# Kernel tuning notes

Measured on AMD Instinct MI355X. Metric: run time of the kernel, lower is better.

## Reference

```python
import jax, jax.numpy as jnp
import numpy as np

B = 524288  # number of mel frames
MEL = 128   # mel bins (hard-coded in module)
D = 64      # code dim
K = 128     # codebook size


def setup_inputs() -> dict:
    key = jax.random.key(0)
    ks = jax.random.split(key, 7)
    return {
        "mel_frame": jax.random.normal(ks[0], (B, MEL), dtype=jnp.float32),
        "W_in": jax.random.normal(ks[1], (D, MEL), dtype=jnp.float32) * 0.05,
        "b_in": jax.random.normal(ks[2], (D,), dtype=jnp.float32) * 0.05,
        "cb0": jax.random.normal(ks[3], (K, D), dtype=jnp.float32),
        "cb1": jax.random.normal(ks[4], (K, D), dtype=jnp.float32),
        "W_out": jax.random.normal(ks[5], (MEL, D), dtype=jnp.float32) * 0.05,
        "b_out": jax.random.normal(ks[6], (MEL,), dtype=jnp.float32) * 0.05,
    }


def reference(mel_frame, W_in, b_in, cb0, cb1, W_out, b_out):
    # encode: project mel -> d, then greedy residual VQ over 2 codebooks
    z = mel_frame @ W_in.T + b_in                      # (B, D)
    residual = z
    z_q = jnp.zeros_like(z)
    idxs = []
    for cb in (cb0, cb1):
        # squared L2 distance without materializing (B, K, D):
        # ||r - c||^2 = ||r||^2 - 2 r.c + ||c||^2  -> (B, K)
        dist = (
            jnp.sum(residual * residual, axis=-1, keepdims=True)
            - 2.0 * (residual @ cb.T)
            + jnp.sum(cb * cb, axis=-1)
        )
        ind = jnp.argmin(dist, axis=-1)                # (B,)
        code = cb[ind]                                 # gather chosen codes (B, D)
        residual = residual - code
        z_q = z_q + code
        idxs.append(ind)
    # decode: sum of selected codes -> project back to mel
    mel = z_q @ W_out.T + b_out                        # (B, MEL)
    return mel, jnp.stack(idxs, axis=-1)
```

## Files before the change

### kernel.cpp

```cpp
#include <hip/hip_runtime.h>
#include <hip/hip_bf16.h>

#define B_ROWS   524288
#define MEL_BINS 128
#define DIM      64
#define KCODES   128

#define WS_WT 0
#define WS_N0 (WS_WT + MEL_BINS*DIM)
#define WS_N1 (WS_N0 + KCODES)
#define WS_T0 (WS_N1 + KCODES)
#define WS_T1 (WS_T0 + KCODES*MEL_BINS)
#define WS_TOT (WS_T1 + KCODES*MEL_BINS)

__device__ __forceinline__ float np_pairwise64_sq(const float* v) {
#pragma clang fp contract(off)
    float r0 = v[0]*v[0], r1 = v[1]*v[1], r2 = v[2]*v[2], r3 = v[3]*v[3];
    float r4 = v[4]*v[4], r5 = v[5]*v[5], r6 = v[6]*v[6], r7 = v[7]*v[7];
#pragma unroll
    for (int i = 8; i < 64; i += 8) {
        r0 += v[i+0]*v[i+0]; r1 += v[i+1]*v[i+1];
        r2 += v[i+2]*v[i+2]; r3 += v[i+3]*v[i+3];
        r4 += v[i+4]*v[i+4]; r5 += v[i+5]*v[i+5];
        r6 += v[i+6]*v[i+6]; r7 += v[i+7]*v[i+7];
    }
    return ((r0 + r1) + (r2 + r3)) + ((r4 + r5) + (r6 + r7));
}

__global__ __launch_bounds__(256) void rvq_precomp(
    const float* __restrict__ W_in, const float* __restrict__ cb0,
    const float* __restrict__ cb1, const float* __restrict__ W_out,
    float* __restrict__ ws)
{
#pragma clang fp contract(off)
    float* WT = ws + WS_WT;
    float* n0 = ws + WS_N0;
    float* n1 = ws + WS_N1;
    float* T0 = ws + WS_T0;
    float* T1 = ws + WS_T1;

    int tid = blockIdx.x * 256 + threadIdx.x;
    if (tid < 16384) {
        int i = tid >> 7, m = tid & 127;
        double a = 0.0;
        for (int d = 0; d < DIM; ++d)
            a = fma((double)cb0[i*DIM + d], (double)W_out[m*DIM + d], a);
        T0[tid] = (float)a;
    } else if (tid < 32768) {
        int t = tid - 16384;
        int i = t >> 7, m = t & 127;
        double a = 0.0;
        for (int d = 0; d < DIM; ++d)
            a = fma((double)cb1[i*DIM + d], (double)W_out[m*DIM + d], a);
        T1[t] = (float)a;
    } else if (tid < 40960) {
        int t = tid - 32768;
        int j = t >> 6, d = t & 63;
        WT[t] = W_in[d*MEL_BINS + j];
    } else if (tid < 41216) {
        int t = tid - 40960;
        const float* cb = (t & 128) ? cb1 : cb0;
        float*       nn = (t & 128) ? n1  : n0;
        int k = t & 127;
        nn[k] = np_pairwise64_sq(cb + k*DIM);
    }
}

__global__ __launch_bounds__(256) void rvq_main(
    const float* __restrict__ mel,
    const float* __restrict__ b_in,
    const float* __restrict__ cb0,
    const float* __restrict__ cb1,
    const float* __restrict__ b_out,
    const float* __restrict__ ws,
    float* __restrict__ out_mel,
    float* __restrict__ out_idx)
{
#pragma clang fp contract(off)
    const float* __restrict__ n0 = ws + WS_N0;
    const float* __restrict__ n1 = ws + WS_N1;
    const float* __restrict__ T0 = ws + WS_T0;
    const float* __restrict__ T1 = ws + WS_T1;

    __shared__ float slds[8192];
    float4* s4 = reinterpret_cast<float4*>(slds);
    const float4* s4c = reinterpret_cast<const float4*>(slds);

    const int tid = threadIdx.x;
    const int b = blockIdx.x * 256 + tid;

    {
        const float4* src = reinterpret_cast<const float4*>(ws + WS_WT);
#pragma unroll
        for (int i = 0; i < 8; ++i) s4[i*256 + tid] = src[i*256 + tid];
    }
    __syncthreads();

    float z[DIM];
#pragma unroll
    for (int d = 0; d < DIM; ++d) z[d] = 0.f;

    const float4* melr = reinterpret_cast<const float4*>(mel + (size_t)b * MEL_BINS);
    for (int jc = 0; jc < MEL_BINS / 4; ++jc) {
        float4 m4 = melr[jc];
#pragma unroll
        for (int seg = 0; seg < 4; ++seg) {
            float mj = (seg == 0) ? m4.x : (seg == 1) ? m4.y : (seg == 2) ? m4.z : m4.w;
            const float4* w4 = s4c + (jc*4 + seg)*16;
#pragma unroll
            for (int q = 0; q < 16; ++q) {
                float4 wv = w4[q];
                z[4*q + 0] = fmaf(wv.x, mj, z[4*q + 0]);
                z[4*q + 1] = fmaf(wv.y, mj, z[4*q + 1]);
                z[4*q + 2] = fmaf(wv.z, mj, z[4*q + 2]);
                z[4*q + 3] = fmaf(wv.w, mj, z[4*q + 3]);
            }
        }
    }
#pragma unroll
    for (int d = 0; d < DIM; ++d) z[d] = z[d] + b_in[d];

    float s0 = z[0]*z[0], s1 = z[1]*z[1], s2 = z[2]*z[2], s3 = z[3]*z[3];
    float s4r = z[4]*z[4], s5 = z[5]*z[5], s6 = z[6]*z[6], s7 = z[7]*z[7];
#pragma unroll
    for (int i = 8; i < 64; i += 8) {
        s0 += z[i+0]*z[i+0]; s1 += z[i+1]*z[i+1];
        s2 += z[i+2]*z[i+2]; s3 += z[i+3]*z[i+3];
        s4r += z[i+4]*z[i+4]; s5 += z[i+5]*z[i+5];
        s6 += z[i+6]*z[i+6]; s7 += z[i+7]*z[i+7];
    }
    float sum_rr = ((s0 + s1) + (s2 + s3)) + ((s4r + s5) + (s6 + s7));

    __syncthreads();
    {
        const float4* src = reinterpret_cast<const float4*>(cb0);
#pragma unroll
        for (int i = 0; i < 8; ++i) s4[i*256 + tid] = src[i*256 + tid];
    }
    __syncthreads();

    float best0 = 3.4e38f; int i0 = 0;
    for (int k = 0; k < KCODES; ++k) {
        const float4* c4 = s4c + k*16;
        float acc = 0.f;
#pragma unroll
        for (int q = 0; q < 16; ++q) {
            float4 cv = c4[q];
            acc = fmaf(cv.x, z[4*q + 0], acc);
            acc = fmaf(cv.y, z[4*q + 1], acc);
            acc = fmaf(cv.z, z[4*q + 2], acc);
            acc = fmaf(cv.w, z[4*q + 3], acc);
        }
        float dist = (sum_rr - 2.0f*acc) + n0[k];
        if (dist < best0) { best0 = dist; i0 = k; }
    }

    __syncthreads();
    {
        const float4* src = reinterpret_cast<const float4*>(cb1);
#pragma unroll
        for (int i = 0; i < 8; ++i) s4[i*256 + tid] = src[i*256 + tid];
    }

    {
        const float* c = cb0 + (size_t)i0 * DIM;
#pragma unroll
        for (int d = 0; d < DIM; ++d) z[d] = z[d] - c[d];
    }

    s0 = z[0]*z[0]; s1 = z[1]*z[1]; s2 = z[2]*z[2]; s3 = z[3]*z[3];
    s4r = z[4]*z[4]; s5 = z[5]*z[5]; s6 = z[6]*z[6]; s7 = z[7]*z[7];
#pragma unroll
    for (int i = 8; i < 64; i += 8) {
        s0 += z[i+0]*z[i+0]; s1 += z[i+1]*z[i+1];
        s2 += z[i+2]*z[i+2]; s3 += z[i+3]*z[i+3];
        s4r += z[i+4]*z[i+4]; s5 += z[i+5]*z[i+5];
        s6 += z[i+6]*z[i+6]; s7 += z[i+7]*z[i+7];
    }
    sum_rr = ((s0 + s1) + (s2 + s3)) + ((s4r + s5) + (s6 + s7));

    __syncthreads();

    float best1 = 3.4e38f; int i1 = 0;
    for (int k = 0; k < KCODES; ++k) {
        const float4* c4 = s4c + k*16;
        float acc = 0.f;
#pragma unroll
        for (int q = 0; q < 16; ++q) {
            float4 cv = c4[q];
            acc = fmaf(cv.x, z[4*q + 0], acc);
            acc = fmaf(cv.y, z[4*q + 1], acc);
            acc = fmaf(cv.z, z[4*q + 2], acc);
            acc = fmaf(cv.w, z[4*q + 3], acc);
        }
        float dist = (sum_rr - 2.0f*acc) + n1[k];
        if (dist < best1) { best1 = dist; i1 = k; }
    }

    const float4* t0r = reinterpret_cast<const float4*>(T0 + (size_t)i0 * MEL_BINS);
    const float4* t1r = reinterpret_cast<const float4*>(T1 + (size_t)i1 * MEL_BINS);
    float4* outr = reinterpret_cast<float4*>(out_mel + (size_t)b * MEL_BINS);
#pragma unroll 4
    for (int q = 0; q < MEL_BINS / 4; ++q) {
        float4 a = t0r[q], c = t1r[q];
        float4 o;
        o.x = a.x + c.x + b_out[4*q + 0];
        o.y = a.y + c.y + b_out[4*q + 1];
        o.z = a.z + c.z + b_out[4*q + 2];
        o.w = a.w + c.w + b_out[4*q + 3];
        outr[q] = o;
    }

    out_idx[2*(size_t)b + 0] = (float)i0;
    out_idx[2*(size_t)b + 1] = (float)i1;
}

extern "C" void kernel_launch(void* const* d_in, const int* in_sizes, int n_in,
                              void* d_out, int out_size, void* d_ws, size_t ws_size,
                              hipStream_t stream)
{
    const float* mel   = (const float*)d_in[0];
    const float* W_in  = (const float*)d_in[1];
    const float* b_in  = (const float*)d_in[2];
    const float* cb0   = (const float*)d_in[3];
    const float* cb1   = (const float*)d_in[4];
    const float* W_out = (const float*)d_in[5];
    const float* b_out = (const float*)d_in[6];

    float* ws      = (float*)d_ws;
    float* out_mel = (float*)d_out;
    float* out_idx = (float*)d_out + (size_t)B_ROWS * MEL_BINS;

    rvq_precomp<<<(WS_TOT + 255) / 256, 256, 0, stream>>>(W_in, cb0, cb1, W_out, ws);
    rvq_main<<<B_ROWS / 256, 256, 0, stream>>>(mel, b_in, cb0, cb1, b_out, ws,
                                               out_mel, out_idx);
}
```

Measured before the change: 570.1 us.

## Compute VQ distances with split-bf16 MFMA and exact fp32 rescoring of candidates

Replaces the per-thread scalar 128-code distance loops with wave-level MFMA matrix multiplies. Residuals and codebooks are split into bf16 hi/lo parts (three MFMA products), and codebooks are stored in a swizzled LDS table. A bitmask of codes within a small margin of the approximate minimum is built by shuffles, and only those candidates are rescored in exact fp32 from global memory. This removes most scalar FMA work, at the cost of many bpermutes and shuffles, divergent rescoring loops, and a fixed margin that must cover the bf16 error.

```diff
diff --git a/kernel.cpp b/kernel.cpp
--- a/kernel.cpp
+++ b/kernel.cpp
@@ -5,6 +5,10 @@
 #define MEL_BINS 128
 #define DIM      64
 #define KCODES   128
+
+typedef short short8 __attribute__((ext_vector_type(8)));
+typedef float f32x4  __attribute__((ext_vector_type(4)));
+typedef unsigned int uint4v __attribute__((ext_vector_type(4)));
 
 #define WS_WT 0
 #define WS_N0 (WS_WT + MEL_BINS*DIM)
@@ -66,6 +70,167 @@
     }
 }
 
+__device__ __forceinline__ unsigned rne16(float x) {
+    unsigned u = __float_as_uint(x);
+    return (u + 0x7fffu + ((u >> 16) & 1u)) >> 16;
+}
+
+__device__ __forceinline__ int vq_step(const float* __restrict__ cbg,
+                                       const float* __restrict__ ng,
+                                       unsigned* tab,
+                                       float (&z)[64], float sum_rr,
+                                       int tid)
+{
+#pragma clang fp contract(off)
+    const int lane = tid & 63;
+    const int c  = lane & 15;
+    const int g  = lane >> 4;
+    const bool gb0 = (lane & 16) != 0;
+    const bool gb1 = (lane & 32) != 0;
+    const int r3  = lane & 3;
+    const int sgl = ((lane >> 2) & 3) << 4;
+    const unsigned bit0 = 1u << c, bit1 = 1u << (16 + c);
+
+    __syncthreads();
+    for (int e = tid; e < 8192; e += 256) {
+        int k = e >> 6, d = e & 63;
+        float v = cbg[e];
+        unsigned hb = rne16(v);
+        float hf = __uint_as_float(hb << 16);
+        unsigned lb = rne16(v - hf);
+        tab[(k << 6) | (d ^ ((k & 7) << 3))] = (hb << 16) | lb;
+    }
+    float nv[8];
+#pragma unroll
+    for (int n = 0; n < 8; ++n) nv[n] = ng[(n << 4) | c];
+    __syncthreads();
+
+    unsigned mybm[4] = {0u, 0u, 0u, 0u};
+
+    for (int T = 0; T < 4; ++T) {
+        const int srcl = ((T << 4) | c) << 2;
+
+        short8 Ah[2], Al[2];
+#pragma unroll
+        for (int ks = 0; ks < 2; ++ks) {
+            unsigned hq[4], lq[4];
+#pragma unroll
+            for (int j = 0; j < 8; ++j) {
+                int p0 = __builtin_amdgcn_ds_bpermute(srcl, __float_as_int(z[32*ks + j]));
+                int p1 = __builtin_amdgcn_ds_bpermute(srcl, __float_as_int(z[32*ks + 8 + j]));
+                int p2 = __builtin_amdgcn_ds_bpermute(srcl, __float_as_int(z[32*ks + 16 + j]));
+                int p3 = __builtin_amdgcn_ds_bpermute(srcl, __float_as_int(z[32*ks + 24 + j]));
+                float av = __int_as_float(gb1 ? (gb0 ? p3 : p2) : (gb0 ? p1 : p0));
+                unsigned hb = rne16(av);
+                float hf = __uint_as_float(hb << 16);
+                unsigned lb = rne16(av - hf);
+                if ((j & 1) == 0) { hq[j >> 1] = hb;       lq[j >> 1] = lb; }
+                else              { hq[j >> 1] |= hb << 16; lq[j >> 1] |= lb << 16; }
+            }
+            uint4v hv = {hq[0], hq[1], hq[2], hq[3]};
+            uint4v lv = {lq[0], lq[1], lq[2], lq[3]};
+            Ah[ks] = __builtin_bit_cast(short8, hv);
+            Al[ks] = __builtin_bit_cast(short8, lv);
+        }
+
+        f32x4 C[8];
+#pragma unroll
+        for (int n = 0; n < 8; ++n) {
+            C[n] = (f32x4){0.f, 0.f, 0.f, 0.f};
+            const int kcol = (n << 4) | c;
+            const int swz = (kcol & 7) << 3;
+#pragma unroll
+            for (int ks = 0; ks < 2; ++ks) {
+                const int d0 = 32*ks + (g << 3);
+                const unsigned* p = &tab[(kcol << 6) | (d0 ^ swz)];
+                uint4v w0 = *(const uint4v*)p;
+                uint4v w1 = *(const uint4v*)(p + 4);
+                unsigned h0 = (w0.x >> 16) | (w0.y & 0xffff0000u);
+                unsigned h1 = (w0.z >> 16) | (w0.w & 0xffff0000u);
+                unsigned h2 = (w1.x >> 16) | (w1.y & 0xffff0000u);
+                unsigned h3 = (w1.z >> 16) | (w1.w & 0xffff0000u);
+                unsigned l0 = (w0.x & 0xffffu) | (w0.y << 16);
+                unsigned l1 = (w0.z & 0xffffu) | (w0.w << 16);
+                unsigned l2 = (w1.x & 0xffffu) | (w1.y << 16);
+                unsigned l3 = (w1.z & 0xffffu) | (w1.w << 16);
+                uint4v bhv = {h0, h1, h2, h3};
+                uint4v blv = {l0, l1, l2, l3};
+                short8 Bh = __builtin_bit_cast(short8, bhv);
+                short8 Bl = __builtin_bit_cast(short8, blv);
+                C[n] = __builtin_amdgcn_mfma_f32_16x16x32_bf16(Ah[ks], Bh, C[n], 0, 0, 0);
+                C[n] = __builtin_amdgcn_mfma_f32_16x16x32_bf16(Ah[ks], Bl, C[n], 0, 0, 0);
+                C[n] = __builtin_amdgcn_mfma_f32_16x16x32_bf16(Al[ks], Bh, C[n], 0, 0, 0);
+            }
+        }
+
+        float thr[4];
+#pragma unroll
+        for (int i = 0; i < 4; ++i) {
+            float m = fmaf(-2.f, C[0][i], nv[0]);
+#pragma unroll
+            for (int n = 1; n < 8; ++n) m = fminf(m, fmaf(-2.f, C[n][i], nv[n]));
+            m = fminf(m, __shfl_xor(m, 1));
+            m = fminf(m, __shfl_xor(m, 2));
+            m = fminf(m, __shfl_xor(m, 4));
+            m = fminf(m, __shfl_xor(m, 8));
+            thr[i] = m + 0.0625f;
+        }
+        unsigned bm[4][4] = {};
+#pragma unroll
+        for (int n = 0; n < 8; ++n) {
+            const unsigned bb = (n & 1) ? bit1 : bit0;
+#pragma unroll
+            for (int i = 0; i < 4; ++i) {
+                float v = fmaf(-2.f, C[n][i], nv[n]);
+                if (v <= thr[i]) bm[i][n >> 1] |= bb;
+            }
+        }
+#pragma unroll
+        for (int i = 0; i < 4; ++i) {
+#pragma unroll
+            for (int w = 0; w < 4; ++w) {
+                unsigned x = bm[i][w];
+                x |= __shfl_xor(x, 1);
+                x |= __shfl_xor(x, 2);
+                x |= __shfl_xor(x, 4);
+                x |= __shfl_xor(x, 8);
+                bm[i][w] = x;
+            }
+        }
+#pragma unroll
+        for (int w = 0; w < 4; ++w) {
+            unsigned t0 = __shfl(bm[0][w], sgl);
+            unsigned t1 = __shfl(bm[1][w], sgl);
+            unsigned t2 = __shfl(bm[2][w], sgl);
+            unsigned t3 = __shfl(bm[3][w], sgl);
+            unsigned vsel = (r3 == 0) ? t0 : (r3 == 1) ? t1 : (r3 == 2) ? t2 : t3;
+            if ((lane >> 4) == T) mybm[w] = vsel;
+        }
+    }
+
+    float best = 3.4e38f; int bi = 0;
+    for (int w = 0; w < 4; ++w) {
+        unsigned u = mybm[w];
+        while (u) {
+            const int k = (w << 5) + __builtin_ctz(u);
+            u &= u - 1;
+            const float4* cr = (const float4*)(cbg + (k << 6));
+            float acc = 0.f;
+#pragma unroll
+            for (int q = 0; q < 16; ++q) {
+                float4 cv = cr[q];
+                acc = fmaf(cv.x, z[4*q + 0], acc);
+                acc = fmaf(cv.y, z[4*q + 1], acc);
+                acc = fmaf(cv.z, z[4*q + 2], acc);
+                acc = fmaf(cv.w, z[4*q + 3], acc);
+            }
+            float dist = (sum_rr - 2.0f*acc) + ng[k];
+            if (dist < best) { best = dist; bi = k; }
+        }
+    }
+    return bi;
+}
+
 __global__ __launch_bounds__(256) void rvq_main(
     const float* __restrict__ mel,
     const float* __restrict__ b_in,
@@ -77,19 +242,18 @@
     float* __restrict__ out_idx)
 {
 #pragma clang fp contract(off)
-    const float* __restrict__ n0 = ws + WS_N0;
-    const float* __restrict__ n1 = ws + WS_N1;
-    const float* __restrict__ T0 = ws + WS_T0;
-    const float* __restrict__ T1 = ws + WS_T1;
-
-    __shared__ float slds[8192];
-    float4* s4 = reinterpret_cast<float4*>(slds);
-    const float4* s4c = reinterpret_cast<const float4*>(slds);
+    const float* __restrict__ n0g = ws + WS_N0;
+    const float* __restrict__ n1g = ws + WS_N1;
+    const float* __restrict__ T0  = ws + WS_T0;
+    const float* __restrict__ T1  = ws + WS_T1;
+
+    __shared__ unsigned tab[8192];
 
     const int tid = threadIdx.x;
     const int b = blockIdx.x * 256 + tid;
 
     {
+        float4* s4 = reinterpret_cast<float4*>(tab);
         const float4* src = reinterpret_cast<const float4*>(ws + WS_WT);
 #pragma unroll
         for (int i = 0; i < 8; ++i) s4[i*256 + tid] = src[i*256 + tid];
@@ -101,6 +265,7 @@
     for (int d = 0; d < DIM; ++d) z[d] = 0.f;
 
     const float4* melr = reinterpret_cast<const float4*>(mel + (size_t)b * MEL_BINS);
+    const float4* s4c = reinterpret_cast<const float4*>(tab);
     for (int jc = 0; jc < MEL_BINS / 4; ++jc) {
         float4 m4 = melr[jc];
 #pragma unroll
@@ -131,43 +296,13 @@
     }
     float sum_rr = ((s0 + s1) + (s2 + s3)) + ((s4r + s5) + (s6 + s7));
 
-    __syncthreads();
+    const int i0 = vq_step(cb0, n0g, tab, z, sum_rr, tid);
+
     {
-        const float4* src = reinterpret_cast<const float4*>(cb0);
-#pragma unroll
-        for (int i = 0; i < 8; ++i) s4[i*256 + tid] = src[i*256 + tid];
-    }
-    __syncthreads();
-
-    float best0 = 3.4e38f; int i0 = 0;
-    for (int k = 0; k < KCODES; ++k) {
-        const float4* c4 = s4c + k*16;
-        float acc = 0.f;
-#pragma unroll
-        for (int q = 0; q < 16; ++q) {
-            float4 cv = c4[q];
-            acc = fmaf(cv.x, z[4*q + 0], acc);
-            acc = fmaf(cv.y, z[4*q + 1], acc);
-            acc = fmaf(cv.z, z[4*q + 2], acc);
-            acc = fmaf(cv.w, z[4*q + 3], acc);
-        }
-        float dist = (sum_rr - 2.0f*acc) + n0[k];
-        if (dist < best0) { best0 = dist; i0 = k; }
-    }
-
-    __syncthreads();
-    {
-        const float4* src = reinterpret_cast<const float4*>(cb1);
-#pragma unroll
-        for (int i = 0; i < 8; ++i) s4[i*256 + tid] = src[i*256 + tid];
-    }
-
-    {
-        const float* c = cb0 + (size_t)i0 * DIM;
-#pragma unroll
-        for (int d = 0; d < DIM; ++d) z[d] = z[d] - c[d];
-    }
-
+        const float* cc = cb0 + (size_t)i0 * DIM;
+#pragma unroll
+        for (int d = 0; d < DIM; ++d) z[d] = z[d] - cc[d];
+    }
     s0 = z[0]*z[0]; s1 = z[1]*z[1]; s2 = z[2]*z[2]; s3 = z[3]*z[3];
     s4r = z[4]*z[4]; s5 = z[5]*z[5]; s6 = z[6]*z[6]; s7 = z[7]*z[7];
 #pragma unroll
@@ -179,35 +314,19 @@
     }
     sum_rr = ((s0 + s1) + (s2 + s3)) + ((s4r + s5) + (s6 + s7));
 
-    __syncthreads();
-
-    float best1 = 3.4e38f; int i1 = 0;
-    for (int k = 0; k < KCODES; ++k) {
-        const float4* c4 = s4c + k*16;
-        float acc = 0.f;
-#pragma unroll
-        for (int q = 0; q < 16; ++q) {
-            float4 cv = c4[q];
-            acc = fmaf(cv.x, z[4*q + 0], acc);
-            acc = fmaf(cv.y, z[4*q + 1], acc);
-            acc = fmaf(cv.z, z[4*q + 2], acc);
-            acc = fmaf(cv.w, z[4*q + 3], acc);
-        }
-        float dist = (sum_rr - 2.0f*acc) + n1[k];
-        if (dist < best1) { best1 = dist; i1 = k; }
-    }
+    const int i1 = vq_step(cb1, n1g, tab, z, sum_rr, tid);
 
     const float4* t0r = reinterpret_cast<const float4*>(T0 + (size_t)i0 * MEL_BINS);
     const float4* t1r = reinterpret_cast<const float4*>(T1 + (size_t)i1 * MEL_BINS);
     float4* outr = reinterpret_cast<float4*>(out_mel + (size_t)b * MEL_BINS);
 #pragma unroll 4
     for (int q = 0; q < MEL_BINS / 4; ++q) {
-        float4 a = t0r[q], c = t1r[q];
+        float4 a = t0r[q], cc = t1r[q];
         float4 o;
-        o.x = a.x + c.x + b_out[4*q + 0];
-        o.y = a.y + c.y + b_out[4*q + 1];
-        o.z = a.z + c.z + b_out[4*q + 2];
-        o.w = a.w + c.w + b_out[4*q + 3];
+        o.x = a.x + cc.x + b_out[4*q + 0];
+        o.y = a.y + cc.y + b_out[4*q + 1];
+        o.z = a.z + cc.z + b_out[4*q + 2];
+        o.w = a.w + cc.w + b_out[4*q + 3];
         outr[q] = o;
     }
 
```

Result: slower. 612.3 us (+7.4%).
